# Kernel tuning notes

Measured on AMD Instinct MI355X. Metric: run time of the kernel, lower is better.

The kernel has to match this reference:

```python
import jax, jax.numpy as jnp
from jax import lax
import numpy as np

NBINS = 50

def _make_filters():
    coords = np.linspace(-1.0, 1.0, 3)
    zz, yy, xx = np.meshgrid(coords, coords, coords, indexing='ij')
    gf = []
    for freq in [2.0, 4.0]:
        for ang in [0.0, np.pi / 4, np.pi / 2, 3 * np.pi / 4]:
            gauss = np.exp(-(xx ** 2 + yy ** 2 + zz ** 2) / 0.5)
            f = gauss * np.cos(freq * (xx * np.cos(ang) + yy * np.sin(ang)))
            f = f - f.mean()
            s = f.std(ddof=1)  # torch std is unbiased
            if s > 1e-8:
                f = f / s
            gf.append(f)
    gf = np.stack(gf)[:, None].astype(np.float32)  # (8,1,3,3,3)
    lf = []
    for axis in range(3):
        for sign in [1, -1]:
            f = np.zeros((3, 3, 3), np.float32)
            f[1, 1, 1] = 1.0
            idx = [1, 1, 1]
            idx[axis] += sign
            f[tuple(idx)] = -1.0
            lf.append(f)
    lf = np.stack(lf)[:, None].astype(np.float32)  # (6,1,3,3,3)
    return gf, lf

def setup_inputs() -> dict:
    key = jax.random.key(0)
    k1, k2 = jax.random.split(key)
    B, D, H, W = 4, 96, 160, 160
    x = jax.random.uniform(k1, (B, 1, D, H, W), jnp.float32, minval=-1.0, maxval=1.0)
    mask = (jax.random.uniform(k2, (B, 1, D, H, W), jnp.float32) > 0.5).astype(jnp.float32)
    gf, lf = _make_filters()
    return {"x": x, "mask": mask, "gabor_filters": jnp.asarray(gf), "lbp_filters": jnp.asarray(lf)}

def _hu_stats(v, mf):
    # v, mf: (B,D,H,W); mf is 0/1 float mask
    n = mf.sum((1, 2, 3))                      # (B,)
    nn = jnp.maximum(n, 1.0)
    mu = (mf * v).sum((1, 2, 3)) / nn
    diff = (v - mu[:, None, None, None]) * mf
    var = (diff ** 2).sum((1, 2, 3)) / jnp.maximum(n - 1.0, 1.0)  # unbiased, like torch .std()
    sigma = jnp.sqrt(var) + 1e-8
    z = diff / sigma[:, None, None, None]
    skew = (z ** 3).sum((1, 2, 3)) / nn
    kurt = (z ** 4).sum((1, 2, 3)) / nn - 3.0
    # histogram over [-1,1] with 50 bins; torch.histc ignores out-of-range, last bin inclusive
    w = mf * ((v >= -1.0) & (v <= 1.0)).astype(v.dtype)
    idx = jnp.clip(jnp.floor((v + 1.0) * (NBINS / 2.0)).astype(jnp.int32), 0, NBINS - 1)
    hist = jax.vmap(lambda i, wb: jnp.zeros((NBINS,), v.dtype).at[i.ravel()].add(wb.ravel()))(idx, w)
    p = hist / (hist.sum(-1, keepdims=True) + 1e-8)
    ent = -(p * jnp.log(p + 1e-8)).sum(-1)
    valid = (n >= 10.0).astype(v.dtype)
    return jnp.stack([mu, sigma, skew, kurt, ent], axis=1) * valid[:, None]  # (B,5)

def _glcm_proxy(v, m):
    # v: (B,D,H,W) float; m: (B,D,H,W) bool
    rows = []
    for axis in range(3):
        a = axis + 1
        sl1 = tuple(slice(None, -1) if i == a else slice(None) for i in range(4))
        sl2 = tuple(slice(1, None) if i == a else slice(None) for i in range(4))
        d = v[sl1] - v[sl2]
        mp = (m[sl1] & m[sl2]).astype(v.dtype)
        s = mp.sum((1, 2, 3))
        ss = jnp.maximum(s, 1.0)
        con = (mp * d * d).sum((1, 2, 3)) / ss
        hom = (mp / (1.0 + d * d)).sum((1, 2, 3)) / ss
        ok = (s >= 4.0).astype(v.dtype)
        rows += [con * ok, hom * ok]
    return jnp.stack(rows, axis=1)  # (B,6)

def _forward(x, mask, gabor_filters, lbp_filters):
    v = x[:, 0]                       # (B,D,H,W)
    m = mask[:, 0] > 0.5              # bool
    mf = m.astype(x.dtype)
    hu = _hu_stats(v, mf)             # (B,5)
    dn = ('NCDHW', 'OIDHW', 'NCDHW')
    pad = [(1, 1)] * 3
    gab = lax.conv_general_dilated(x, gabor_filters, (1, 1, 1), pad, dimension_numbers=dn)
    lung_vol = jnp.clip(mask.sum((2, 3, 4)), 1.0, None)      # (B,1)
    gab_feat = jnp.abs(gab * mask).sum((2, 3, 4)) / lung_vol  # (B,8)
    lbp = lax.conv_general_dilated(x, lbp_filters, (1, 1, 1), pad, dimension_numbers=dn)
    lbp = lbp * mask
    lbp_feat = ((lbp > 0).astype(x.dtype) * mask).sum((2, 3, 4)) / lung_vol  # (B,6)
    glcm = _glcm_proxy(v, m)          # (B,6)
    return jnp.concatenate([hu, gab_feat, lbp_feat, glcm], axis=1)  # (B,25)

def reference(x, mask, gabor_filters, lbp_filters):
    return _forward(x, mask, gabor_filters, lbp_filters)
```

## Files before the change

kernel.cpp:

```cpp
#include <hip/hip_runtime.h>
#include <math.h>

#define B_    4
#define D_    96
#define H_    160
#define W_    160
#define HW_   (H_ * W_)
#define NVOX  (D_ * H_ * W_)
#define NBINS 50
#define NQR   28
#define CPB   256
#define PART_F (B_ * NQR * CPB)
#define HIST_U PART_F
#define WQ_F   (PART_F + 200)
#define TS    36

typedef float f2 __attribute__((ext_vector_type(2)));

__device__ __forceinline__ float rfl(float v) {
    return __uint_as_float(__builtin_amdgcn_readfirstlane(__float_as_uint(v)));
}

__device__ __forceinline__ void gload_lds(const float* g, float* l) {
    __builtin_amdgcn_global_load_lds(
        (const __attribute__((address_space(1))) unsigned int*)(g),
        (__attribute__((address_space(3))) unsigned int*)(l),
        4, 0, 0);
}

__global__ __launch_bounds__(64) void radiomics_weights(
    const float* __restrict__ gf, const float* __restrict__ lf,
    float* __restrict__ ws)
{
    const int lane = threadIdx.x;
    __shared__ float sCs[8][5], sR[8], sMO[8], sMC[8];
    if (lane < 8) {
        const int f = lane;
        float O9[9], C9[9];
        float mC = 0.f, mO = 0.f;
#pragma unroll
        for (int k = 0; k < 9; ++k) {
            O9[k] = gf[f * 27 + k];
            C9[k] = gf[f * 27 + 9 + k];
            mC += C9[k]; mO += O9[k];
        }
        mC *= (1.f / 9.f); mO *= (1.f / 9.f);
        float cov = 0.f, var = 0.f;
#pragma unroll
        for (int k = 0; k < 9; ++k) {
            float c = C9[k] - mC, o = O9[k] - mO;
            cov += c * o; var += c * c;
        }
        sR[f] = cov / var; sMO[f] = mO; sMC[f] = mC;
#pragma unroll
        for (int j = 0; j < 4; ++j) sCs[f][j] = 0.5f * (C9[j] + C9[8 - j]);
        sCs[f][4] = C9[4];
    }
    __syncthreads();
    if (lane == 0) {
        float* wq = ws + WQ_F;
        float gz0 = 0.f;
        for (int f = 0; f < 8; ++f) gz0 += sR[f];
        gz0 *= 0.125f;
        wq[0] = gz0;
        float df[8];
        for (int f = 0; f < 8; ++f) df[f] = sMO[f] - gz0 * sMC[f];
        for (int F = 0; F < 2; ++F) {
            const int f0 = 4 * F, f1 = 4 * F + 1, f2 = 4 * F + 2, f3 = 4 * F + 3;
            float* g = wq + 1 + 11 * F;
            g[0]  = 0.5f * (df[f0] + df[f2]);
            g[1]  = 0.5f * (sCs[f0][0] + sCs[f2][0]);
            g[2]  = 0.5f * (sCs[f0][2] + sCs[f2][2]);
            g[3]  = 0.5f * (sCs[f0][4] + sCs[f2][4]);
            g[4]  = 0.5f * (sCs[f0][1] + sCs[f2][3]);
            g[5]  = 0.5f * (sCs[f0][3] + sCs[f2][1]);
            g[6]  = 0.5f * (df[f1] + df[f3]);
            g[7]  = 0.25f * (sCs[f1][1] + sCs[f1][3]
                           + sCs[f3][1] + sCs[f3][3]);
            g[8]  = 0.5f * (sCs[f1][4] + sCs[f3][4]);
            g[9]  = 0.5f * (sCs[f1][0] + sCs[f3][2]);
            g[10] = 0.5f * (sCs[f1][2] + sCs[f3][0]);
        }
    }
    unsigned int* gh = (unsigned int*)ws + HIST_U;
    for (int i = lane; i < B_ * NBINS; i += 64) gh[i] = 0u;
}

#define STAGE(bi, zp) do {                                                  \
    const float* px_ = xbb + (size_t)(zp) * HW_;                            \
    const float* pm_ = mbb + (size_t)(zp) * HW_;                            \
    _Pragma("unroll")                                                       \
    for (int j_ = 0; j_ < 3; ++j_) {                                        \
        gload_lds(px_ + xsrc[j_], &xs[bi][lbase + 256 * j_]);               \
        gload_lds(pm_ + msrc[j_], &msd[bi][lbase + 256 * j_]);              \
    }                                                                       \
} while (0)

#define RDX(s, bi) do {                                                     \
    _Pragma("unroll")                                                       \
    for (int r_ = 0; r_ < 3; ++r_) {                                        \
        f2 a_  = *(const f2*)&xs[bi][(ty + r_) * TS + 2 * tx];              \
        f2 b2_ = *(const f2*)&xs[bi][(ty + r_) * TS + 2 * tx + 2];          \
        Xw[s][r_][0] = a_.x;  Xw[s][r_][1] = a_.y;                          \
        Xw[s][r_][2] = b2_.x; Xw[s][r_][3] = b2_.y;                         \
    }                                                                       \
} while (0)

#define FINISH(s, bzv) do {                                                 \
    if ((bzv) == 0.f) {                                                     \
        _Pragma("unroll")                                                   \
        for (int r_ = 0; r_ < 3; ++r_)                                      \
            _Pragma("unroll")                                               \
            for (int c_ = 0; c_ < 4; ++c_) Xw[s][r_][c_] = 0.f;             \
        S9[s][0] = S9[s][1] = 0.f;                                          \
    } else {                                                                \
        _Pragma("unroll")                                                   \
        for (int c_ = 0; c_ < 4; ++c_) {                                    \
            Xw[s][0][c_] *= bndRow0; Xw[s][2][c_] *= bndRow2;               \
        }                                                                   \
        _Pragma("unroll")                                                   \
        for (int r_ = 0; r_ < 3; ++r_) {                                    \
            Xw[s][r_][0] *= bndL; Xw[s][r_][3] *= bndR;                     \
        }                                                                   \
        float cs0_ = Xw[s][0][0] + Xw[s][1][0] + Xw[s][2][0];               \
        float cs1_ = Xw[s][0][1] + Xw[s][1][1] + Xw[s][2][1];               \
        float cs2_ = Xw[s][0][2] + Xw[s][1][2] + Xw[s][2][2];               \
        float cs3_ = Xw[s][0][3] + Xw[s][1][3] + Xw[s][2][3];               \
        S9[s][0] = cs0_ + cs1_ + cs2_;                                      \
        S9[s][1] = cs1_ + cs2_ + cs3_;                                      \
    }                                                                       \
} while (0)

__global__ __launch_bounds__(256) void radiomics_main(
    const float* __restrict__ x, const float* __restrict__ mask,
    float* __restrict__ ws)
{
    __shared__ float xs[4][768];
    __shared__ float msd[4][768];
    __shared__ unsigned int shist[4 * NBINS];
    __shared__ float xred[4][NQR];

    const int tid = threadIdx.x;
    const int tx = tid & 15, ty = tid >> 4;
    const int lane = tid & 63, wid = tid >> 6;
    const int lbase = __builtin_amdgcn_readfirstlane(tid & ~63);

    for (int i = tid; i < 4 * NBINS; i += 256) shist[i] = 0u;

    const float* wq = ws + WQ_F;
    const float gz0 = rfl(wq[0]);
    float gco[22];
#pragma unroll
    for (int i = 0; i < 22; ++i) gco[i] = rfl(wq[1 + i]);

    const int c = blockIdx.x;
    const int b = blockIdx.z;
    int t, z0, nz;
    if (c < 36) {
        t  = c / 6;
        const int ci = c - 6 * t;
        z0 = 16 * ci; nz = 16;
    } else {
        const int c2 = c - 36;
        const int ti = c2 / 5;
        const int ci = c2 - 5 * ti;
        t = 6 + ti;
        if (ci == 0) { z0 = 0; nz = 16; }
        else         { z0 = 20 * ci - 4; nz = 20; }
    }
    const int ngroups = nz >> 2;

    const int gx0t = (t % 5) * 32;
    const int gy0t = (t / 5) * 16;
    const int gx = gx0t + tx * 2;
    const int gy = gy0t + ty;

    const float* __restrict__ xbb = x    + (size_t)b * NVOX;
    const float* __restrict__ mbb = mask + (size_t)b * NVOX;

    int xsrc[3], msrc[3];
#pragma unroll
    for (int j = 0; j < 3; ++j) {
        int idx = tid + 256 * j;
        int row = idx / TS;
        int col = idx - row * TS;
        int gr = gy0t - 1 + row; gr = gr < 0 ? 0 : (gr > H_ - 1 ? H_ - 1 : gr);
        int gc = gx0t - 1 + col; gc = gc < 0 ? 0 : (gc > W_ - 1 ? W_ - 1 : gc);
        xsrc[j] = gr * W_ + gc;
        int mr = gy0t + row; mr = mr > H_ - 1 ? H_ - 1 : mr;
        int mcc = gx0t + col; mcc = mcc > W_ - 1 ? W_ - 1 : mcc;
        msrc[j] = mr * W_ + mcc;
    }

    const float bndRow0 = (gy > 0) ? 1.f : 0.f;
    const float bndRow2 = (gy + 1 < H_) ? 1.f : 0.f;
    const float bndL = (gx > 0) ? 1.f : 0.f;
    const float bndR = (gx + 2 < W_) ? 1.f : 0.f;
    const float bym = bndRow2, bxm = bndR;

    float Xw[4][3][4];
    float S9[4][2];
    float Mq[2][2];
    f2    myq[2];
    float mxq[2];
    float acc[NQR];
#pragma unroll
    for (int q = 0; q < NQR; ++q) acc[q] = 0.f;

    STAGE(3, (z0 > 0) ? z0 - 1 : 0);
    STAGE(0, z0);
    STAGE(1, z0 + 1);
    asm volatile("s_waitcnt vmcnt(0)" ::: "memory");
    __builtin_amdgcn_s_barrier();
    __builtin_amdgcn_sched_barrier(0);

    if (z0 == 0) {
#pragma unroll
        for (int r = 0; r < 3; ++r)
#pragma unroll
            for (int cc = 0; cc < 4; ++cc) Xw[3][r][cc] = 0.f;
        S9[3][0] = S9[3][1] = 0.f;
    } else {
        RDX(3, 3);
        FINISH(3, 1.f);
    }
    RDX(0, 0);
    FINISH(0, 1.f);
    {
        f2 cm0 = *(const f2*)&msd[0][ty * TS + 2 * tx];
        Mq[0][0] = (cm0.x > 0.5f) ? 1.f : 0.f;
        Mq[0][1] = (cm0.y > 0.5f) ? 1.f : 0.f;
        myq[0] = *(const f2*)&msd[0][(ty + 1) * TS + 2 * tx];
        mxq[0] = msd[0][ty * TS + 2 * tx + 2];
    }

    int z = z0;
#pragma unroll 1
    for (int g = 0; g < ngroups; ++g) {
#pragma unroll
        for (int j = 0; j < 4; ++j) {
            const int cs = j & 3;
            const int c0 = (j + 3) & 3;
            const int c2 = (j + 1) & 3;
            const int bn = (j + 1) & 3;
            const int bs = (j + 2) & 3;
            const int cur = j & 1, nxt = cur ^ 1;

            const int zs = (z + 2 < D_) ? z + 2 : D_ - 1;
            STAGE(bs, zs);
            asm volatile("s_waitcnt vmcnt(6)" ::: "memory");
            __builtin_amdgcn_s_barrier();
            __builtin_amdgcn_sched_barrier(0);

            const float bzn = (z + 1 < D_) ? 1.f : 0.f;
            RDX(c2, bn);
            FINISH(c2, bzn);
            {
                f2 cmm = *(const f2*)&msd[bn][ty * TS + 2 * tx];
                Mq[nxt][0] = (cmm.x * bzn > 0.5f) ? 1.f : 0.f;
                Mq[nxt][1] = (cmm.y * bzn > 0.5f) ? 1.f : 0.f;
                myq[nxt] = *(const f2*)&msd[bn][(ty + 1) * TS + 2 * tx];
                mxq[nxt] = msd[bn][ty * TS + 2 * tx + 2];
            }

            float T6[3][4];
#pragma unroll
            for (int r = 0; r < 3; ++r)
#pragma unroll
                for (int cc = 0; cc < 4; ++cc)
                    T6[r][cc] = fmaf(gz0, Xw[c0][r][cc] + Xw[c2][r][cc], Xw[cs][r][cc]);

            const f2 my2 = myq[cur];
            const float mxs = mxq[cur];

#pragma unroll
            for (int q = 0; q < 2; ++q) {
                const float v  = Xw[cs][1][q + 1];
                const float mc = Mq[cur][q];

                acc[0] += mc;
                float mv  = mc * v;  acc[1] += mv;
                float mv2 = mv * v;  acc[2] += mv2;
                float mv3 = mv2 * v; acc[3] += mv3;
                acc[4] += mv3 * v;

                if (mc > 0.5f && v >= -1.f && v <= 1.f) {
                    int bi = (int)floorf((v + 1.f) * (NBINS * 0.5f));
                    bi = min(max(bi, 0), NBINS - 1);
                    atomicAdd(&shist[(tid >> 6) * NBINS + bi], 1u);
                }

                float P0 = T6[0][q]     + T6[2][q + 2];
                float P1 = T6[0][q + 1] + T6[2][q + 1];
                float P2 = T6[0][q + 2] + T6[2][q];
                float P3 = T6[1][q]     + T6[1][q + 2];
                float ctrv = T6[1][q + 1];
                float S2 = S9[c0][q] + S9[c2][q];
                float Qv = P1 + P3;
#pragma unroll
                for (int F = 0; F < 2; ++F) {
                    const float dfA = gco[F*11+0], c0s = gco[F*11+1];
                    const float c2s = gco[F*11+2], c4s = gco[F*11+3];
                    const float cu  = gco[F*11+4], cw  = gco[F*11+5];
                    const float dfB = gco[F*11+6], ct  = gco[F*11+7];
                    const float ce  = gco[F*11+8], ca  = gco[F*11+9];
                    const float cb  = gco[F*11+10];
                    float E = dfA * S2;
                    E = fmaf(c0s, P0, E); E = fmaf(c2s, P2, E); E = fmaf(c4s, ctrv, E);
                    float r0   = fmaf(cu, P1, fmaf(cw, P3, E));
                    float r90  = fmaf(cw, P1, fmaf(cu, P3, E));
                    float G = fmaf(ct, Qv, dfB * S2);
                    G = fmaf(ce, ctrv, G);
                    float r45  = fmaf(ca, P0, fmaf(cb, P2, G));
                    float r135 = fmaf(cb, P0, fmaf(ca, P2, G));
                    acc[5 + 4*F + 0] = fmaf(fabsf(r0),   mc, acc[5 + 4*F + 0]);
                    acc[5 + 4*F + 1] = fmaf(fabsf(r45),  mc, acc[5 + 4*F + 1]);
                    acc[5 + 4*F + 2] = fmaf(fabsf(r90),  mc, acc[5 + 4*F + 2]);
                    acc[5 + 4*F + 3] = fmaf(fabsf(r135), mc, acc[5 + 4*F + 3]);
                }

                const float nb[6] = { Xw[c2][1][q + 1], Xw[c0][1][q + 1],
                                      Xw[cs][2][q + 1], Xw[cs][0][q + 1],
                                      Xw[cs][1][q + 2], Xw[cs][1][q] };
#pragma unroll
                for (int f = 0; f < 6; ++f)
                    acc[13 + f] += (v > nb[f]) ? mc : 0.f;

                {
                    float mp = mc * Mq[nxt][q];
                    float d = v - Xw[c2][1][q + 1], dd = d * d;
                    acc[19] += mp;
                    acc[22] = fmaf(mp, dd, acc[22]);
                    acc[25] = fmaf(mp, __builtin_amdgcn_rcpf(1.f + dd), acc[25]);
                }
                {
                    float mr = (q == 0) ? my2.x : my2.y;
                    float mp = mc * (((mr > 0.5f) ? 1.f : 0.f) * bym);
                    float d = v - Xw[cs][2][q + 1], dd = d * d;
                    acc[20] += mp;
                    acc[23] = fmaf(mp, dd, acc[23]);
                    acc[26] = fmaf(mp, __builtin_amdgcn_rcpf(1.f + dd), acc[26]);
                }
                {
                    float mnr = (q == 0) ? Mq[cur][1] : (((mxs > 0.5f) ? 1.f : 0.f) * bxm);
                    float mp = mc * mnr;
                    float d = v - Xw[cs][1][q + 2], dd = d * d;
                    acc[21] += mp;
                    acc[24] = fmaf(mp, dd, acc[24]);
                    acc[27] = fmaf(mp, __builtin_amdgcn_rcpf(1.f + dd), acc[27]);
                }
            }
            ++z;
        }
    }

#pragma unroll
    for (int q = 0; q < NQR; ++q) {
        float sm = acc[q];
#pragma unroll
        for (int o = 32; o > 0; o >>= 1)
            sm += __shfl_down(sm, o, 64);
        acc[q] = sm;
    }
    if (lane == 0) {
#pragma unroll
        for (int q = 0; q < NQR; ++q) xred[wid][q] = acc[q];
    }
    __syncthreads();

    if (tid < NQR) {
        float v = xred[0][tid] + xred[1][tid] + xred[2][tid] + xred[3][tid];
        ws[((size_t)b * NQR + tid) * CPB + c] = v;
    } else if (tid < NQR + NBINS) {
        int h = tid - NQR;
        unsigned int cnt = shist[h] + shist[NBINS + h]
                         + shist[2 * NBINS + h] + shist[3 * NBINS + h];
        unsigned int* ghist = (unsigned int*)ws + HIST_U;
        if (cnt) atomicAdd(&ghist[b * NBINS + h], cnt);
    }
}

__global__ __launch_bounds__(512) void radiomics_tail(
    const float* __restrict__ ws, float* __restrict__ out)
{
    __shared__ double fin[NQR];
    __shared__ double hcnt[NBINS];
    __shared__ double entp[NBINS];
    __shared__ double sh_hsum;
    const int b = blockIdx.x, tid = threadIdx.x;
    const int wave = tid >> 6, lane = tid & 63;

    for (int q = wave; q < NQR; q += 8) {
        const float* p = ws + ((size_t)b * NQR + q) * CPB;
        double s = 0.0;
#pragma unroll
        for (int k = 0; k < 4; ++k)
            s += (double)p[lane + 64 * k];
#pragma unroll
        for (int o = 32; o > 0; o >>= 1)
            s += __shfl_down(s, o, 64);
        if (lane == 0) fin[q] = s;
    }
    if (tid < NBINS)
        hcnt[tid] = (double)(((const unsigned int*)ws)[HIST_U + b * NBINS + tid]);
    __syncthreads();

    if (tid == 0) {
        double h = 0.0;
        for (int k = 0; k < NBINS; ++k) h += hcnt[k];
        sh_hsum = h + 1e-8;
    }
    __syncthreads();

    if (tid < NBINS) {
        double p = hcnt[tid] / sh_hsum;
        entp[tid] = -p * log(p + 1e-8);
    }
    __syncthreads();

    if (tid == 0) {
        const double n  = fin[0];
        const double nn = fmax(n, 1.0);
        const double s1 = fin[1], s2 = fin[2], s3 = fin[3], s4 = fin[4];
        const double mu = s1 / nn;
        const double M2 = s2 - 2.0 * mu * s1 + mu * mu * n;
        const double M3 = s3 - 3.0 * mu * s2 + 3.0 * mu * mu * s1 - mu * mu * mu * n;
        const double M4 = s4 - 4.0 * mu * s3 + 6.0 * mu * mu * s2
                          - 4.0 * mu * mu * mu * s1 + mu * mu * mu * mu * n;
        const double var   = M2 / fmax(n - 1.0, 1.0);
        const double sigma = sqrt(var) + 1e-8;
        const double skew  = M3 / (sigma * sigma * sigma) / nn;
        const double kurt  = M4 / (sigma * sigma * sigma * sigma) / nn - 3.0;

        double ent = 0.0;
        for (int k = 0; k < NBINS; ++k) ent += entp[k];

        const double valid = (n >= 10.0) ? 1.0 : 0.0;
        float* ob = out + b * 25;
        ob[0] = (float)(mu * valid);
        ob[1] = (float)(sigma * valid);
        ob[2] = (float)(skew * valid);
        ob[3] = (float)(kurt * valid);
        ob[4] = (float)(ent * valid);

        const double lung = fmax(n, 1.0);
        for (int f = 0; f < 8; ++f) ob[5 + f]  = (float)(fin[5 + f] / lung);
        for (int f = 0; f < 6; ++f) ob[13 + f] = (float)(fin[13 + f] / lung);

        for (int ax = 0; ax < 3; ++ax) {
            double s  = fin[19 + ax];
            double ss = fmax(s, 1.0);
            double ok = (s >= 4.0) ? 1.0 : 0.0;
            ob[19 + 2 * ax]     = (float)(fin[22 + ax] / ss * ok);
            ob[19 + 2 * ax + 1] = (float)(fin[25 + ax] / ss * ok);
        }
    }
}

extern "C" void kernel_launch(void* const* d_in, const int* in_sizes, int n_in,
                              void* d_out, int out_size, void* d_ws, size_t ws_size,
                              hipStream_t stream)
{
    const float* x    = (const float*)d_in[0];
    const float* mask = (const float*)d_in[1];
    const float* gf   = (const float*)d_in[2];
    const float* lf   = (const float*)d_in[3];
    float* out = (float*)d_out;
    float* ws  = (float*)d_ws;

    radiomics_weights<<<1, 64, 0, stream>>>(gf, lf, ws);
    radiomics_main<<<dim3(256, 1, B_), 256, 0, stream>>>(x, mask, ws);
    radiomics_tail<<<B_, 512, 0, stream>>>(ws, out);
}
```

Measured before the change: 166.4 us.

## Fuse weight prep into main kernel, use per-wave LDS tiles, load mask directly

```diff
diff --git a/kernel.cpp b/kernel.cpp
--- a/kernel.cpp
+++ b/kernel.cpp
@@ -9,11 +9,9 @@
 #define NVOX  (D_ * H_ * W_)
 #define NBINS 50
 #define NQR   28
+#define NQ    78
 #define CPB   256
-#define PART_F (B_ * NQR * CPB)
-#define HIST_U PART_F
-#define WQ_F   (PART_F + 200)
-#define TS    36
+#define LASTP ((D_ - 1) * HW_)
 
 typedef float f2 __attribute__((ext_vector_type(2)));
 
@@ -28,79 +26,19 @@
         4, 0, 0);
 }
 
-__global__ __launch_bounds__(64) void radiomics_weights(
-    const float* __restrict__ gf, const float* __restrict__ lf,
-    float* __restrict__ ws)
-{
-    const int lane = threadIdx.x;
-    __shared__ float sCs[8][5], sR[8], sMO[8], sMC[8];
-    if (lane < 8) {
-        const int f = lane;
-        float O9[9], C9[9];
-        float mC = 0.f, mO = 0.f;
-#pragma unroll
-        for (int k = 0; k < 9; ++k) {
-            O9[k] = gf[f * 27 + k];
-            C9[k] = gf[f * 27 + 9 + k];
-            mC += C9[k]; mO += O9[k];
-        }
-        mC *= (1.f / 9.f); mO *= (1.f / 9.f);
-        float cov = 0.f, var = 0.f;
-#pragma unroll
-        for (int k = 0; k < 9; ++k) {
-            float c = C9[k] - mC, o = O9[k] - mO;
-            cov += c * o; var += c * c;
-        }
-        sR[f] = cov / var; sMO[f] = mO; sMC[f] = mC;
-#pragma unroll
-        for (int j = 0; j < 4; ++j) sCs[f][j] = 0.5f * (C9[j] + C9[8 - j]);
-        sCs[f][4] = C9[4];
-    }
-    __syncthreads();
-    if (lane == 0) {
-        float* wq = ws + WQ_F;
-        float gz0 = 0.f;
-        for (int f = 0; f < 8; ++f) gz0 += sR[f];
-        gz0 *= 0.125f;
-        wq[0] = gz0;
-        float df[8];
-        for (int f = 0; f < 8; ++f) df[f] = sMO[f] - gz0 * sMC[f];
-        for (int F = 0; F < 2; ++F) {
-            const int f0 = 4 * F, f1 = 4 * F + 1, f2 = 4 * F + 2, f3 = 4 * F + 3;
-            float* g = wq + 1 + 11 * F;
-            g[0]  = 0.5f * (df[f0] + df[f2]);
-            g[1]  = 0.5f * (sCs[f0][0] + sCs[f2][0]);
-            g[2]  = 0.5f * (sCs[f0][2] + sCs[f2][2]);
-            g[3]  = 0.5f * (sCs[f0][4] + sCs[f2][4]);
-            g[4]  = 0.5f * (sCs[f0][1] + sCs[f2][3]);
-            g[5]  = 0.5f * (sCs[f0][3] + sCs[f2][1]);
-            g[6]  = 0.5f * (df[f1] + df[f3]);
-            g[7]  = 0.25f * (sCs[f1][1] + sCs[f1][3]
-                           + sCs[f3][1] + sCs[f3][3]);
-            g[8]  = 0.5f * (sCs[f1][4] + sCs[f3][4]);
-            g[9]  = 0.5f * (sCs[f1][0] + sCs[f3][2]);
-            g[10] = 0.5f * (sCs[f1][2] + sCs[f3][0]);
-        }
-    }
-    unsigned int* gh = (unsigned int*)ws + HIST_U;
-    for (int i = lane; i < B_ * NBINS; i += 64) gh[i] = 0u;
-}
-
 #define STAGE(bi, zp) do {                                                  \
     const float* px_ = xbb + (size_t)(zp) * HW_;                            \
-    const float* pm_ = mbb + (size_t)(zp) * HW_;                            \
     _Pragma("unroll")                                                       \
-    for (int j_ = 0; j_ < 3; ++j_) {                                        \
-        gload_lds(px_ + xsrc[j_], &xs[bi][lbase + 256 * j_]);               \
-        gload_lds(pm_ + msrc[j_], &msd[bi][lbase + 256 * j_]);              \
-    }                                                                       \
+    for (int k_ = 0; k_ < 4; ++k_)                                          \
+        gload_lds(px_ + xsrc4[k_], &xs[bi][widu][64 * k_]);                 \
 } while (0)
 
-#define RDX(s, bi) do {                                                     \
+#define RDXL(s, bi) do {                                                    \
+    const float* xw_ = &xs[bi][widu][0];                                    \
     _Pragma("unroll")                                                       \
     for (int r_ = 0; r_ < 3; ++r_) {                                        \
-        f2 a_  = *(const f2*)&xs[bi][(ty + r_) * TS + 2 * tx];              \
-        f2 b2_ = *(const f2*)&xs[bi][(ty + r_) * TS + 2 * tx + 2];          \
+        f2 a_  = *(const f2*)(xw_ + (tyw + r_) * 36 + 2 * tx);              \
+        f2 b2_ = *(const f2*)(xw_ + (tyw + r_) * 36 + 2 * tx + 2);          \
         Xw[s][r_][0] = a_.x;  Xw[s][r_][1] = a_.y;                          \
         Xw[s][r_][2] = b2_.x; Xw[s][r_][3] = b2_.y;                         \
     }                                                                       \
@@ -133,25 +71,70 @@
 
 __global__ __launch_bounds__(256) void radiomics_main(
     const float* __restrict__ x, const float* __restrict__ mask,
-    float* __restrict__ ws)
+    const float* __restrict__ gf, float* __restrict__ ws)
 {
-    __shared__ float xs[4][768];
-    __shared__ float msd[4][768];
+    __shared__ float xs[4][4][256];
+    __shared__ float sgf[8 * 27];
     __shared__ unsigned int shist[4 * NBINS];
     __shared__ float xred[4][NQR];
 
     const int tid = threadIdx.x;
     const int tx = tid & 15, ty = tid >> 4;
+    const int tyw = ty & 3;
     const int lane = tid & 63, wid = tid >> 6;
-    const int lbase = __builtin_amdgcn_readfirstlane(tid & ~63);
-
+    const int widu = __builtin_amdgcn_readfirstlane(wid);
+
+    for (int i = tid; i < 8 * 27; i += 256) sgf[i] = gf[i];
     for (int i = tid; i < 4 * NBINS; i += 256) shist[i] = 0u;
-
-    const float* wq = ws + WQ_F;
-    const float gz0 = rfl(wq[0]);
-    float gco[22];
-#pragma unroll
-    for (int i = 0; i < 22; ++i) gco[i] = rfl(wq[1 + i]);
+    __syncthreads();
+
+    float gz0, gco[22];
+    {
+        float asum = 0.f, mOa[8], mCa[8], Cs[8][5];
+#pragma unroll
+        for (int f = 0; f < 8; ++f) {
+            float C9[9];
+            float mC = 0.f, mO = 0.f;
+#pragma unroll
+            for (int k = 0; k < 9; ++k) {
+                C9[k] = sgf[f * 27 + 9 + k];
+                mC += C9[k];
+                mO += sgf[f * 27 + k];
+            }
+            mC *= (1.f / 9.f); mO *= (1.f / 9.f);
+            float cov = 0.f, var = 0.f;
+#pragma unroll
+            for (int k = 0; k < 9; ++k) {
+                float c = C9[k] - mC, o = sgf[f * 27 + k] - mO;
+                cov += c * o; var += c * c;
+            }
+            asum += cov / var; mOa[f] = mO; mCa[f] = mC;
+#pragma unroll
+            for (int j = 0; j < 4; ++j)
+                Cs[f][j] = rfl(0.5f * (C9[j] + C9[8 - j]));
+            Cs[f][4] = rfl(C9[4]);
+        }
+        gz0 = rfl(asum * 0.125f);
+        float df[8];
+#pragma unroll
+        for (int f = 0; f < 8; ++f) df[f] = rfl(mOa[f] - gz0 * mCa[f]);
+#pragma unroll
+        for (int F = 0; F < 2; ++F) {
+            const int f0 = 4 * F, f1 = 4 * F + 1, f2 = 4 * F + 2, f3 = 4 * F + 3;
+            float* g = gco + 11 * F;
+            g[0]  = rfl(0.5f * (df[f0] + df[f2]));
+            g[1]  = rfl(0.5f * (Cs[f0][0] + Cs[f2][0]));
+            g[2]  = rfl(0.5f * (Cs[f0][2] + Cs[f2][2]));
+            g[3]  = rfl(0.5f * (Cs[f0][4] + Cs[f2][4]));
+            g[4]  = rfl(0.5f * (Cs[f0][1] + Cs[f2][3]));
+            g[5]  = rfl(0.5f * (Cs[f0][3] + Cs[f2][1]));
+            g[6]  = rfl(0.5f * (df[f1] + df[f3]));
+            g[7]  = rfl(0.25f * (Cs[f1][1] + Cs[f1][3] + Cs[f3][1] + Cs[f3][3]));
+            g[8]  = rfl(0.5f * (Cs[f1][4] + Cs[f3][4]));
+            g[9]  = rfl(0.5f * (Cs[f1][0] + Cs[f3][2]));
+            g[10] = rfl(0.5f * (Cs[f1][2] + Cs[f3][0]));
+        }
+    }
 
     const int c = blockIdx.x;
     const int b = blockIdx.z;
@@ -174,28 +157,31 @@
     const int gy0t = (t / 5) * 16;
     const int gx = gx0t + tx * 2;
     const int gy = gy0t + ty;
+    const int gy0w = gy0t + 4 * wid;
 
     const float* __restrict__ xbb = x    + (size_t)b * NVOX;
     const float* __restrict__ mbb = mask + (size_t)b * NVOX;
 
-    int xsrc[3], msrc[3];
-#pragma unroll
-    for (int j = 0; j < 3; ++j) {
-        int idx = tid + 256 * j;
-        int row = idx / TS;
-        int col = idx - row * TS;
-        int gr = gy0t - 1 + row; gr = gr < 0 ? 0 : (gr > H_ - 1 ? H_ - 1 : gr);
+    int xsrc4[4];
+#pragma unroll
+    for (int k = 0; k < 4; ++k) {
+        int idx = 64 * k + lane;
+        int row = idx / 36;
+        int col = idx - 36 * row;
+        int gr = gy0w - 1 + row; gr = gr < 0 ? 0 : (gr > H_ - 1 ? H_ - 1 : gr);
         int gc = gx0t - 1 + col; gc = gc < 0 ? 0 : (gc > W_ - 1 ? W_ - 1 : gc);
-        xsrc[j] = gr * W_ + gc;
-        int mr = gy0t + row; mr = mr > H_ - 1 ? H_ - 1 : mr;
-        int mcc = gx0t + col; mcc = mcc > W_ - 1 ? W_ - 1 : mcc;
-        msrc[j] = mr * W_ + mcc;
+        xsrc4[k] = gr * W_ + gc;
     }
 
     const float bndRow0 = (gy > 0) ? 1.f : 0.f;
     const float bndRow2 = (gy + 1 < H_) ? 1.f : 0.f;
     const float bndL = (gx > 0) ? 1.f : 0.f;
     const float bndR = (gx + 2 < W_) ? 1.f : 0.f;
+    const int gy2 = (gy + 1 < H_) ? gy + 1 : H_ - 1;
+    const int xR  = (gx + 2 < W_) ? gx + 2 : W_ - 1;
+    const int moff  = gy * W_ + gx;
+    const int myoff = gy2 * W_ + gx;
+    const int mxoff = gy * W_ + xR;
     const float bym = bndRow2, bxm = bndR;
 
     float Xw[4][3][4];
@@ -211,7 +197,6 @@
     STAGE(0, z0);
     STAGE(1, z0 + 1);
     asm volatile("s_waitcnt vmcnt(0)" ::: "memory");
-    __builtin_amdgcn_s_barrier();
     __builtin_amdgcn_sched_barrier(0);
 
     if (z0 == 0) {
@@ -221,20 +206,21 @@
             for (int cc = 0; cc < 4; ++cc) Xw[3][r][cc] = 0.f;
         S9[3][0] = S9[3][1] = 0.f;
     } else {
-        RDX(3, 3);
+        RDXL(3, 3);
         FINISH(3, 1.f);
     }
-    RDX(0, 0);
+    RDXL(0, 0);
     FINISH(0, 1.f);
     {
-        f2 cm0 = *(const f2*)&msd[0][ty * TS + 2 * tx];
+        f2 cm0 = *(const f2*)(mbb + (size_t)z0 * HW_ + moff);
         Mq[0][0] = (cm0.x > 0.5f) ? 1.f : 0.f;
         Mq[0][1] = (cm0.y > 0.5f) ? 1.f : 0.f;
-        myq[0] = *(const f2*)&msd[0][(ty + 1) * TS + 2 * tx];
-        mxq[0] = msd[0][ty * TS + 2 * tx + 2];
-    }
-
-    int z = z0;
+        myq[0] = *(const f2*)(mbb + (size_t)z0 * HW_ + myoff);
+        mxq[0] = mbb[(size_t)z0 * HW_ + mxoff];
+    }
+
+    int z  = z0;
+    int zc = z0 * HW_;
 #pragma unroll 1
     for (int g = 0; g < ngroups; ++g) {
 #pragma unroll
@@ -246,22 +232,24 @@
             const int bs = (j + 2) & 3;
             const int cur = j & 1, nxt = cur ^ 1;
 
+            const int zn = (zc + HW_ < NVOX) ? zc + HW_ : LASTP;
+            f2 cmm = *(const f2*)(mbb + zn + moff);
+            f2 myn = *(const f2*)(mbb + zn + myoff);
+            float mxn = mbb[zn + mxoff];
+            __builtin_amdgcn_sched_barrier(0);
             const int zs = (z + 2 < D_) ? z + 2 : D_ - 1;
             STAGE(bs, zs);
-            asm volatile("s_waitcnt vmcnt(6)" ::: "memory");
-            __builtin_amdgcn_s_barrier();
             __builtin_amdgcn_sched_barrier(0);
+            asm volatile("s_waitcnt vmcnt(7)" ::: "memory");
+            __builtin_amdgcn_sched_barrier(0);
 
             const float bzn = (z + 1 < D_) ? 1.f : 0.f;
-            RDX(c2, bn);
+            RDXL(c2, bn);
             FINISH(c2, bzn);
-            {
-                f2 cmm = *(const f2*)&msd[bn][ty * TS + 2 * tx];
-                Mq[nxt][0] = (cmm.x * bzn > 0.5f) ? 1.f : 0.f;
-                Mq[nxt][1] = (cmm.y * bzn > 0.5f) ? 1.f : 0.f;
-                myq[nxt] = *(const f2*)&msd[bn][(ty + 1) * TS + 2 * tx];
-                mxq[nxt] = msd[bn][ty * TS + 2 * tx + 2];
-            }
+            Mq[nxt][0] = (cmm.x * bzn > 0.5f) ? 1.f : 0.f;
+            Mq[nxt][1] = (cmm.y * bzn > 0.5f) ? 1.f : 0.f;
+            myq[nxt] = myn;
+            mxq[nxt] = mxn;
 
             float T6[3][4];
 #pragma unroll
@@ -287,7 +275,7 @@
                 if (mc > 0.5f && v >= -1.f && v <= 1.f) {
                     int bi = (int)floorf((v + 1.f) * (NBINS * 0.5f));
                     bi = min(max(bi, 0), NBINS - 1);
-                    atomicAdd(&shist[(tid >> 6) * NBINS + bi], 1u);
+                    atomicAdd(&shist[widu * NBINS + bi], 1u);
                 }
 
                 float P0 = T6[0][q]     + T6[2][q + 2];
@@ -350,7 +338,7 @@
                     acc[27] = fmaf(mp, __builtin_amdgcn_rcpf(1.f + dd), acc[27]);
                 }
             }
-            ++z;
+            ++z; zc += HW_;
         }
     }
 
@@ -368,30 +356,29 @@
     }
     __syncthreads();
 
+    float* wsb = ws + (size_t)b * NQ * CPB;
     if (tid < NQR) {
         float v = xred[0][tid] + xred[1][tid] + xred[2][tid] + xred[3][tid];
-        ws[((size_t)b * NQR + tid) * CPB + c] = v;
-    } else if (tid < NQR + NBINS) {
+        wsb[tid * CPB + c] = v;
+    } else if (tid < NQ) {
         int h = tid - NQR;
         unsigned int cnt = shist[h] + shist[NBINS + h]
                          + shist[2 * NBINS + h] + shist[3 * NBINS + h];
-        unsigned int* ghist = (unsigned int*)ws + HIST_U;
-        if (cnt) atomicAdd(&ghist[b * NBINS + h], cnt);
+        wsb[tid * CPB + c] = (float)cnt;
     }
 }
 
 __global__ __launch_bounds__(512) void radiomics_tail(
     const float* __restrict__ ws, float* __restrict__ out)
 {
-    __shared__ double fin[NQR];
-    __shared__ double hcnt[NBINS];
+    __shared__ double fin[NQ];
     __shared__ double entp[NBINS];
     __shared__ double sh_hsum;
     const int b = blockIdx.x, tid = threadIdx.x;
     const int wave = tid >> 6, lane = tid & 63;
 
-    for (int q = wave; q < NQR; q += 8) {
-        const float* p = ws + ((size_t)b * NQR + q) * CPB;
+    for (int q = wave; q < NQ; q += 8) {
+        const float* p = ws + ((size_t)b * NQ + q) * CPB;
         double s = 0.0;
 #pragma unroll
         for (int k = 0; k < 4; ++k)
@@ -401,19 +388,17 @@
             s += __shfl_down(s, o, 64);
         if (lane == 0) fin[q] = s;
     }
-    if (tid < NBINS)
-        hcnt[tid] = (double)(((const unsigned int*)ws)[HIST_U + b * NBINS + tid]);
     __syncthreads();
 
     if (tid == 0) {
         double h = 0.0;
-        for (int k = 0; k < NBINS; ++k) h += hcnt[k];
+        for (int k = 0; k < NBINS; ++k) h += fin[NQR + k];
         sh_hsum = h + 1e-8;
     }
     __syncthreads();
 
     if (tid < NBINS) {
-        double p = hcnt[tid] / sh_hsum;
+        double p = fin[NQR + tid] / sh_hsum;
         entp[tid] = -p * log(p + 1e-8);
     }
     __syncthreads();
@@ -464,11 +449,9 @@
     const float* x    = (const float*)d_in[0];
     const float* mask = (const float*)d_in[1];
     const float* gf   = (const float*)d_in[2];
-    const float* lf   = (const float*)d_in[3];
     float* out = (float*)d_out;
     float* ws  = (float*)d_ws;
 
-    radiomics_weights<<<1, 64, 0, stream>>>(gf, lf, ws);
-    radiomics_main<<<dim3(256, 1, B_), 256, 0, stream>>>(x, mask, ws);
+    radiomics_main<<<dim3(256, 1, B_), 256, 0, stream>>>(x, mask, gf, ws);
     radiomics_tail<<<B_, 512, 0, stream>>>(ws, out);
 }
```

Result: slower. 206.9 us (+24.3%).
